# Kernel tuning notes

Measured on AMD Instinct MI355X. Metric: run time of the kernel, lower is better.

The kernel has to match this reference:

```python
import jax, jax.numpy as jnp
import numpy as np

N_NODES = 50000
N_EDGES = 800000
N_GRAPHS = 128
IN_CH, HIDDEN, OUT_CH = 16, 64, 2


def gcn_conv(x, src, dst, W, b, n_nodes):
    """GCNConv: add self-loops, sym-normalized adjacency scatter-add, linear."""
    h = x @ W  # [N, H]
    loop = jnp.arange(n_nodes, dtype=src.dtype)
    s = jnp.concatenate([src, loop])  # [E+N]
    d = jnp.concatenate([dst, loop])
    deg = jax.ops.segment_sum(jnp.ones_like(d, dtype=h.dtype), d, num_segments=n_nodes)
    dinv = jnp.where(deg > 0, jax.lax.rsqrt(deg), 0.0)  # deg^{-1/2}
    norm = dinv[s] * dinv[d]  # [E+N]
    msg = h[s] * norm[:, None]  # gather + scale, [E+N, H]
    out = jax.ops.segment_sum(msg, d, num_segments=n_nodes)  # scatter-add
    return out + b


def global_mean_pool(x, batch, n_graphs):
    sums = jax.ops.segment_sum(x, batch, num_segments=n_graphs)
    cnts = jax.ops.segment_sum(jnp.ones((x.shape[0],), x.dtype), batch, num_segments=n_graphs)
    return sums / jnp.maximum(cnts, 1.0)[:, None]


def setup_inputs() -> dict:
    key = jax.random.key(0)
    ks = jax.random.split(key, 10)
    x = jax.random.normal(ks[0], (N_NODES, IN_CH), dtype=jnp.float32)
    edge_index = jax.random.randint(ks[1], (2, N_EDGES), 0, N_NODES, dtype=jnp.int64)
    batch = jnp.sort(jax.random.randint(ks[2], (N_NODES,), 0, N_GRAPHS, dtype=jnp.int64))
    def glorot(k, shp):
        lim = float(np.sqrt(6.0 / (shp[0] + shp[1])))
        return jax.random.uniform(k, shp, jnp.float32, -lim, lim)
    W1 = glorot(ks[3], (IN_CH, HIDDEN))
    b1 = jnp.zeros((HIDDEN,), jnp.float32)
    W2 = glorot(ks[4], (HIDDEN, HIDDEN))
    b2 = jnp.zeros((HIDDEN,), jnp.float32)
    Wc = glorot(ks[5], (HIDDEN, OUT_CH))
    bc = jnp.zeros((OUT_CH,), jnp.float32)
    return {"x": x, "edge_index": edge_index, "batch": batch,
            "W1": W1, "b1": b1, "W2": W2, "b2": b2, "Wc": Wc, "bc": bc}


def reference(x, edge_index, batch, W1, b1, W2, b2, Wc, bc):
    src, dst = edge_index[0], edge_index[1]
    n = x.shape[0]
    h = jax.nn.relu(gcn_conv(x, src, dst, W1, b1, n))
    # dropout p=0.3 is identity in eval mode
    h = jax.nn.relu(gcn_conv(h, src, dst, W2, b2, n))
    g = global_mean_pool(h, batch, N_GRAPHS)  # [G, H]
    return g @ Wc + bc  # [G, out_channels]
```

## Files before the change

### kernel.cpp

```cpp
#include <hip/hip_runtime.h>
#include <hip/hip_bf16.h>

#define N_NODES 50000
#define N_EDGES 800000
#define N_GRAPHS 128
#define IN_CH 16
#define HIDDEN 64
#define OUT_CH 2

#define BSHIFT 7
#define BNODES 128
#define NB ((N_NODES + BNODES - 1) / BNODES)
#define BCAP 3072
#define ECHUNK 4096
#define EB ((N_EDGES + ECHUNK - 1) / ECHUNK)
#define MAXK 12
#define EPT 16
#define WT1_LD 18
#define AGG_LD 72
#define W2T_ENT (HIDDEN * AGG_LD)

typedef __attribute__((ext_vector_type(8))) short bf16x8;
typedef __attribute__((ext_vector_type(4))) float f32x4;

__device__ __forceinline__ float bf2f(unsigned short u) {
    return __uint_as_float(((unsigned)u) << 16);
}
__device__ __forceinline__ unsigned short f2bf(float f) {
    __hip_bfloat16 h = __float2bfloat16(f);
    return *reinterpret_cast<unsigned short*>(&h);
}


__global__ void bucket_scatter_kernel(const int* __restrict__ src, const int* __restrict__ dst,
                                      int* __restrict__ bh, int* __restrict__ bh2,
                                      int* __restrict__ pairs,
                                      const float* __restrict__ W2, unsigned short* __restrict__ w2t) {
    __shared__ int lh[NB];
    __shared__ int lstart[NB];
    __shared__ int spair[256];
    int t = threadIdx.x;
    if (blockIdx.x == 0) {
        for (int i = t; i < HIDDEN * HIDDEN; i += 256) {
            int k = i >> 6, c = i & 63;
            w2t[c * AGG_LD + k] = f2bf(W2[i]);
        }
    }
    for (int i = t; i < NB; i += 256) lh[i] = 0;
    __syncthreads();

    int base = blockIdx.x * ECHUNK;
    int nE = N_EDGES - base;
    if (nE > ECHUNK) nE = ECHUNK;

    int ed[EPT], es[EPT];
#pragma unroll
    for (int k = 0; k < EPT; k++) {
        int i = k * 256 + t;
        if (i < nE) {
            ed[k] = dst[base + i];
            es[k] = src[base + i];
        } else {
            ed[k] = -1;
            es[k] = 0;
        }
    }
#pragma unroll
    for (int k = 0; k < EPT; k++)
        if ((unsigned)ed[k] < N_NODES) atomicAdd(&lh[ed[k] >> BSHIFT], 1);
    __syncthreads();

    int a0 = (2 * t < NB) ? lh[2 * t] : 0;
    int a1 = (2 * t + 1 < NB) ? lh[2 * t + 1] : 0;
    spair[t] = a0 + a1;
    __syncthreads();
    for (int off = 1; off < 256; off <<= 1) {
        int u = (t >= off) ? spair[t - off] : 0;
        __syncthreads();
        spair[t] += u;
        __syncthreads();
    }
    int ex = spair[t] - (a0 + a1);
    if (2 * t < NB) lstart[2 * t] = ex;
    if (2 * t + 1 < NB) lstart[2 * t + 1] = ex + a0;
    __syncthreads();

    for (int i = t; i < NB; i += 256) {
        bh[i * EB + blockIdx.x] = lh[i];
        bh2[i * EB + blockIdx.x] = base + lstart[i];
        lh[i] = 0;
    }
    __syncthreads();

#pragma unroll
    for (int k = 0; k < EPT; k++) {
        if ((unsigned)ed[k] < N_NODES) {
            int b = ed[k] >> BSHIFT;
            int r = atomicAdd(&lh[b], 1);
            pairs[base + lstart[b] + r] = (es[k] << BSHIFT) | (ed[k] & (BNODES - 1));
        }
    }
}


__global__ void bucket_csr_kernel(const int* __restrict__ pairs, const int* __restrict__ bh,
                                  const int* __restrict__ bh2,
                                  int* __restrict__ csr, int* __restrict__ rowptr,
                                  int* __restrict__ cnt_node, float* __restrict__ dinv,
                                  const float* __restrict__ x, unsigned short* __restrict__ xs,
                                  float* __restrict__ sums, float* __restrict__ cntg) {
    __shared__ int segaddr[EB];
    __shared__ int pref[EB];
    __shared__ int ptmp[256];
    __shared__ int lcnt[BNODES];
    __shared__ int lsc[BNODES];
    __shared__ int lrow[BNODES];
    __shared__ float sdv[BNODES];
    int b = blockIdx.x;
    int t = threadIdx.x;

    if (b == 0) {
        for (int i = t; i < N_GRAPHS * HIDDEN; i += 256) sums[i] = 0.0f;
        if (t < N_GRAPHS) cntg[t] = 0.0f;
    }

    int cntv = (t < EB) ? bh[b * EB + t] : 0;
    if (t < EB) segaddr[t] = bh2[b * EB + t];
    if (t < BNODES) lcnt[t] = 0;
    ptmp[t] = cntv;
    __syncthreads();
    for (int off = 1; off < 256; off <<= 1) {
        int u = (t >= off) ? ptmp[t - off] : 0;
        __syncthreads();
        ptmp[t] += u;
        __syncthreads();
    }
    if (t < EB) pref[t] = ptmp[t];
    __syncthreads();
    int K = pref[EB - 1];
    if (K > BCAP) K = BCAP;

    int myp[MAXK], myr[MAXK];
#pragma unroll
    for (int k = 0; k < MAXK; k++) {
        int i = k * 256 + t;
        myp[k] = -1;
        if (i < K) {
            int lo = 0, hi = EB - 1;
            while (lo < hi) {
                int mid = (lo + hi) >> 1;
                if (pref[mid] > i) hi = mid; else lo = mid + 1;
            }
            int excl = (lo > 0) ? pref[lo - 1] : 0;
            int p = pairs[segaddr[lo] + (i - excl)];
            myp[k] = p;
            myr[k] = atomicAdd(&lcnt[p & (BNODES - 1)], 1);
        }
    }
    __syncthreads();
    if (t < BNODES) lsc[t] = lcnt[t];
    __syncthreads();
    for (int off = 1; off < BNODES; off <<= 1) {
        int u = (t >= off && t < BNODES) ? lsc[t - off] : 0;
        __syncthreads();
        if (t < BNODES) lsc[t] += u;
        __syncthreads();
    }
    int bstart = b * BCAP;
    if (t < BNODES) {
        int ex = lsc[t] - lcnt[t];
        lrow[t] = ex;
        float dv = rsqrtf((float)(lcnt[t] + 1));
        sdv[t] = dv;
        int n = b * BNODES + t;
        if (n < N_NODES) {
            rowptr[n] = bstart + ex;
            cnt_node[n] = lcnt[t];
            dinv[n] = dv;
        }
    }
    __syncthreads();
#pragma unroll
    for (int k = 0; k < MAXK; k++) {
        if (myp[k] >= 0)
            csr[bstart + lrow[myp[k] & (BNODES - 1)] + myr[k]] = myp[k] >> BSHIFT;
    }
    for (int i = t; i < BNODES * IN_CH; i += 256) {
        int nl = i >> 4;
        int n = b * BNODES + nl;
        if (n < N_NODES) xs[n * IN_CH + (i & 15)] = f2bf(sdv[nl] * x[n * IN_CH + (i & 15)]);
    }
}


__global__ void fused_l1_kernel(const unsigned short* __restrict__ xs, const int* __restrict__ csr_src,
                                const int* __restrict__ rowptr, const int* __restrict__ cnt,
                                const float* __restrict__ dinv, const float* __restrict__ W,
                                const float* __restrict__ b, __hip_bfloat16* __restrict__ h) {
    __shared__ float sWT[HIDDEN * WT1_LD];
    __shared__ float sx[16 * IN_CH];
    int t = threadIdx.x;
    for (int i = t; i < IN_CH * HIDDEN; i += 512) {
        int k = i >> 6, c = i & 63;
        sWT[c * WT1_LD + k] = W[i];
    }

    int n0 = blockIdx.x * 16;
    int w = t >> 6;
    int lane = t & 63;
    int e16 = lane >> 2;
    int cc = (lane & 3) * 4;

    int lens[2], starts[2];
#pragma unroll
    for (int q = 0; q < 2; q++) {
        int n = n0 + w * 2 + q;
        lens[q] = cnt[n];
        starts[q] = rowptr[n];
    }

    int sidxv[2][2];
    float msk[2][2];
#pragma unroll
    for (int q = 0; q < 2; q++) {
        int last = lens[q] - 1;
        int lastc = last < 0 ? 0 : last;
        int sg = lens[q] > 0 ? -1 : 0;
#pragma unroll
        for (int k = 0; k < 2; k++) {
            int j = e16 + 16 * k;
            int jj = j <= last ? j : lastc;
            msk[q][k] = (j <= last) ? 1.0f : 0.0f;
            sidxv[q][k] = csr_src[starts[q] + jj] & sg;
        }
    }
    ushort4 raw[2][2];
#pragma unroll
    for (int q = 0; q < 2; q++)
#pragma unroll
        for (int k = 0; k < 2; k++)
            raw[q][k] = *(const ushort4*)&xs[sidxv[q][k] * IN_CH + cc];

#pragma unroll
    for (int q = 0; q < 2; q++) {
        int row = w * 2 + q;
        int n = n0 + row;
        int len = lens[q];
        float4 acc = make_float4(0.f, 0.f, 0.f, 0.f);
#pragma unroll
        for (int k = 0; k < 2; k++) {
            float m = msk[q][k];
            acc.x += m * bf2f(raw[q][k].x);
            acc.y += m * bf2f(raw[q][k].y);
            acc.z += m * bf2f(raw[q][k].z);
            acc.w += m * bf2f(raw[q][k].w);
        }
        if (len > 32) {
            int last = len - 1;
            int start = starts[q];
            int iters = (len + 31) >> 5;
            for (int m2 = 1; m2 < iters; m2++) {
                int base2 = m2 * 32 + e16;
#pragma unroll
                for (int k = 0; k < 2; k++) {
                    int j = base2 + 16 * k;
                    int jj = j <= last ? j : last;
                    float m = j <= last ? 1.0f : 0.0f;
                    int s = csr_src[start + jj];
                    ushort4 xv = *(const ushort4*)&xs[s * IN_CH + cc];
                    acc.x += m * bf2f(xv.x);
                    acc.y += m * bf2f(xv.y);
                    acc.z += m * bf2f(xv.z);
                    acc.w += m * bf2f(xv.w);
                }
            }
        }
#pragma unroll
        for (int m = 4; m <= 32; m <<= 1) {
            acc.x += __shfl_xor(acc.x, m, 64);
            acc.y += __shfl_xor(acc.y, m, 64);
            acc.z += __shfl_xor(acc.z, m, 64);
            acc.w += __shfl_xor(acc.w, m, 64);
        }
        if (lane < 4) {
            float dn = dinv[n];
            ushort4 xsv = *(const ushort4*)&xs[n * IN_CH + cc];
            float4 v;
            v.x = dn * (acc.x + bf2f(xsv.x));
            v.y = dn * (acc.y + bf2f(xsv.y));
            v.z = dn * (acc.z + bf2f(xsv.z));
            v.w = dn * (acc.w + bf2f(xsv.w));
            *(float4*)&sx[row * IN_CH + cc] = v;
        }
    }
    __syncthreads();

    int c = t & 63;
    float bias = b[c];
#pragma unroll
    for (int nb = 0; nb < 2; nb++) {
        int row = nb * 8 + w;
        int n = n0 + row;
        float acch = bias;
#pragma unroll
        for (int k4 = 0; k4 < IN_CH; k4 += 4) {
            float4 a = *(const float4*)&sx[row * IN_CH + k4];
            float2 w0 = *(const float2*)&sWT[c * WT1_LD + k4];
            float2 w1 = *(const float2*)&sWT[c * WT1_LD + k4 + 2];
            acch += a.x * w0.x + a.y * w0.y + a.z * w1.x + a.w * w1.y;
        }
        float v = acch > 0.0f ? acch : 0.0f;
        h[n * HIDDEN + c] = __float2bfloat16(dinv[n] * v);
    }
}


__global__ void fused_l2_kernel(const __hip_bfloat16* __restrict__ h, const int* __restrict__ csr_src,
                                const int* __restrict__ rowptr, const int* __restrict__ cnt,
                                const float* __restrict__ dinv, const unsigned short* __restrict__ w2t,
                                const float* __restrict__ b, const int* __restrict__ batch,
                                float* __restrict__ sums, float* __restrict__ cntg) {
    __shared__ unsigned short sW[W2T_ENT];
    __shared__ unsigned short sagg[16 * AGG_LD];
    int t = threadIdx.x;
    {
        const uint4* wp = (const uint4*)w2t;
        uint4* sWv = (uint4*)sW;
#pragma unroll
        for (int i = 0; i < 2; i++) {
            int idx = i * 512 + t;
            if (idx < W2T_ENT / 8) sWv[idx] = wp[idx];
        }
    }

    int n0 = blockIdx.x * 16;
    int w = t >> 6;
    int lane = t & 63;
    int e8 = lane >> 3;
    int cc8 = (lane & 7) * 8;
    const unsigned short* hu = (const unsigned short*)h;

    int lens[2], starts[2];
#pragma unroll
    for (int q = 0; q < 2; q++) {
        int n = n0 + w * 2 + q;
        lens[q] = cnt[n];
        starts[q] = rowptr[n];
    }

    int sidxv[2][4];
    float msk[2][4];
#pragma unroll
    for (int q = 0; q < 2; q++) {
        int last = lens[q] - 1;
        int lastc = last < 0 ? 0 : last;
        int sg = lens[q] > 0 ? -1 : 0;
#pragma unroll
        for (int k = 0; k < 4; k++) {
            int j = e8 + 8 * k;
            int jj = j <= last ? j : lastc;
            msk[q][k] = (j <= last) ? 1.0f : 0.0f;
            sidxv[q][k] = csr_src[starts[q] + jj] & sg;
        }
    }
    uint4 raw[2][4];
#pragma unroll
    for (int q = 0; q < 2; q++)
#pragma unroll
        for (int k = 0; k < 4; k++)
            raw[q][k] = *(const uint4*)&hu[sidxv[q][k] * HIDDEN + cc8];

#pragma unroll
    for (int q = 0; q < 2; q++) {
        int row = w * 2 + q;
        int n = n0 + row;
        int len = lens[q];
        float4 alo = make_float4(0.f, 0.f, 0.f, 0.f);
        float4 ahi = make_float4(0.f, 0.f, 0.f, 0.f);
#pragma unroll
        for (int k = 0; k < 4; k++) {
            float m = msk[q][k];
            uint4 r = raw[q][k];
            alo.x += m * __uint_as_float(r.x << 16);
            alo.y += m * __uint_as_float(r.x & 0xffff0000u);
            alo.z += m * __uint_as_float(r.y << 16);
            alo.w += m * __uint_as_float(r.y & 0xffff0000u);
            ahi.x += m * __uint_as_float(r.z << 16);
            ahi.y += m * __uint_as_float(r.z & 0xffff0000u);
            ahi.z += m * __uint_as_float(r.w << 16);
            ahi.w += m * __uint_as_float(r.w & 0xffff0000u);
        }
        if (len > 32) {
            int last = len - 1;
            int start = starts[q];
            int iters = (len + 31) >> 5;
            for (int m2 = 1; m2 < iters; m2++) {
                int base2 = m2 * 32 + e8;
#pragma unroll
                for (int k = 0; k < 4; k++) {
                    int j = base2 + 8 * k;
                    int jj = j <= last ? j : last;
                    float m = j <= last ? 1.0f : 0.0f;
                    int s = csr_src[start + jj];
                    uint4 r = *(const uint4*)&hu[s * HIDDEN + cc8];
                    alo.x += m * __uint_as_float(r.x << 16);
                    alo.y += m * __uint_as_float(r.x & 0xffff0000u);
                    alo.z += m * __uint_as_float(r.y << 16);
                    alo.w += m * __uint_as_float(r.y & 0xffff0000u);
                    ahi.x += m * __uint_as_float(r.z << 16);
                    ahi.y += m * __uint_as_float(r.z & 0xffff0000u);
                    ahi.z += m * __uint_as_float(r.w << 16);
                    ahi.w += m * __uint_as_float(r.w & 0xffff0000u);
                }
            }
        }
#pragma unroll
        for (int m = 8; m <= 32; m <<= 1) {
            alo.x += __shfl_xor(alo.x, m, 64);
            alo.y += __shfl_xor(alo.y, m, 64);
            alo.z += __shfl_xor(alo.z, m, 64);
            alo.w += __shfl_xor(alo.w, m, 64);
            ahi.x += __shfl_xor(ahi.x, m, 64);
            ahi.y += __shfl_xor(ahi.y, m, 64);
            ahi.z += __shfl_xor(ahi.z, m, 64);
            ahi.w += __shfl_xor(ahi.w, m, 64);
        }
        if (lane < 8) {
            uint4 sv = *(const uint4*)&hu[n * HIDDEN + cc8];
            float dn = dinv[n];
            ushort4 o0, o1;
            o0.x = f2bf(dn * (alo.x + __uint_as_float(sv.x << 16)));
            o0.y = f2bf(dn * (alo.y + __uint_as_float(sv.x & 0xffff0000u)));
            o0.z = f2bf(dn * (alo.z + __uint_as_float(sv.y << 16)));
            o0.w = f2bf(dn * (alo.w + __uint_as_float(sv.y & 0xffff0000u)));
            o1.x = f2bf(dn * (ahi.x + __uint_as_float(sv.z << 16)));
            o1.y = f2bf(dn * (ahi.y + __uint_as_float(sv.z & 0xffff0000u)));
            o1.z = f2bf(dn * (ahi.z + __uint_as_float(sv.w << 16)));
            o1.w = f2bf(dn * (ahi.w + __uint_as_float(sv.w & 0xffff0000u)));
            *(ushort4*)&sagg[row * AGG_LD + cc8] = o0;
            *(ushort4*)&sagg[row * AGG_LD + cc8 + 4] = o1;
        }
    }
    __syncthreads();

    if (w < 4) {
        int quad = lane >> 4;
        int col = lane & 15;
        int cch = w * 16 + col;
        bf16x8 a0 = *(const bf16x8*)&sagg[col * AGG_LD + quad * 8];
        bf16x8 a1 = *(const bf16x8*)&sagg[col * AGG_LD + 32 + quad * 8];
        bf16x8 b0 = *(const bf16x8*)&sW[cch * AGG_LD + quad * 8];
        bf16x8 b1 = *(const bf16x8*)&sW[cch * AGG_LD + 32 + quad * 8];
        f32x4 d = {0.f, 0.f, 0.f, 0.f};
        d = __builtin_amdgcn_mfma_f32_16x16x32_bf16(a0, b0, d, 0, 0, 0);
        d = __builtin_amdgcn_mfma_f32_16x16x32_bf16(a1, b1, d, 0, 0, 0);
        float bias = b[cch];
        float v[4];
#pragma unroll
        for (int r = 0; r < 4; r++) {
            float z = d[r] + bias;
            v[r] = z > 0.0f ? z : 0.0f;
        }

        int glo = batch[n0];
        int ghi = batch[n0 + 15];
        if (glo == ghi) {
            float s4 = (v[0] + v[1]) + (v[2] + v[3]);
            s4 += __shfl_xor(s4, 16, 64);
            s4 += __shfl_xor(s4, 32, 64);
            if (quad == 0) atomicAdd(&sums[glo * HIDDEN + cch], s4);
            if (t == 0) atomicAdd(&cntg[glo], 16.0f);
        } else {
#pragma unroll
            for (int r = 0; r < 4; r++) {
                int g = batch[n0 + quad * 4 + r];
                if ((unsigned)g < N_GRAPHS) atomicAdd(&sums[g * HIDDEN + cch], v[r]);
            }
            if (w == 0 && col == 0) {
#pragma unroll
                for (int r = 0; r < 4; r++) {
                    int g = batch[n0 + quad * 4 + r];
                    if ((unsigned)g < N_GRAPHS) atomicAdd(&cntg[g], 1.0f);
                }
            }
        }
    }
}


__global__ void head_kernel(const float* __restrict__ sums, const float* __restrict__ cntg,
                            const float* __restrict__ Wc, const float* __restrict__ bc,
                            float* __restrict__ out) {
    int t = blockIdx.x * blockDim.x + threadIdx.x;
    if (t >= N_GRAPHS * OUT_CH) return;
    int g = t >> 1;
    int o = t & 1;
    float inv = 1.0f / fmaxf(cntg[g], 1.0f);
    float acc = bc[o];
#pragma unroll
    for (int k = 0; k < HIDDEN; k++) acc += sums[g * HIDDEN + k] * inv * Wc[k * OUT_CH + o];
    out[t] = acc;
}


extern "C" void kernel_launch(void* const* d_in, const int* in_sizes, int n_in,
                              void* d_out, int out_size, void* d_ws, size_t ws_size,
                              hipStream_t stream) {
    const float* x  = (const float*)d_in[0];
    const int* ei   = (const int*)d_in[1];
    const int* bat  = (const int*)d_in[2];
    const float* W1 = (const float*)d_in[3];
    const float* b1 = (const float*)d_in[4];
    const float* W2 = (const float*)d_in[5];
    const float* b2 = (const float*)d_in[6];
    const float* Wc = (const float*)d_in[7];
    const float* bc = (const float*)d_in[8];
    float* out = (float*)d_out;

    const int* src = ei;
    const int* dst = ei + N_EDGES;

    char* ws = (char*)d_ws;
    size_t off = 0;
    auto carve = [&](size_t nbytes) {
        char* p = ws + off;
        off += (nbytes + 255) & ~(size_t)255;
        return p;
    };
    float* sums     = (float*)carve(N_GRAPHS * HIDDEN * sizeof(float));
    float* cntg     = (float*)carve(N_GRAPHS * sizeof(float));
    unsigned short* w2t = (unsigned short*)carve(W2T_ENT * sizeof(unsigned short));
    int*   bh       = (int*)carve((size_t)NB * EB * sizeof(int));
    int*   bh2      = (int*)carve((size_t)NB * EB * sizeof(int));
    int*   pairs    = (int*)carve((size_t)EB * ECHUNK * sizeof(int));
    int*   csr      = (int*)carve((size_t)NB * BCAP * sizeof(int));
    int*   rowptr   = (int*)carve(N_NODES * sizeof(int));
    int*   cnt_node = (int*)carve(N_NODES * sizeof(int));
    float* dinv     = (float*)carve(N_NODES * sizeof(float));
    unsigned short* xs = (unsigned short*)carve((size_t)N_NODES * IN_CH * sizeof(unsigned short));
    __hip_bfloat16* bufA = (__hip_bfloat16*)carve((size_t)N_NODES * HIDDEN * sizeof(__hip_bfloat16));
    (void)ws_size;

    const int node16Blk = (N_NODES + 15) / 16;

    bucket_scatter_kernel<<<EB, 256, 0, stream>>>(src, dst, bh, bh2, pairs, W2, w2t);
    bucket_csr_kernel<<<NB, 256, 0, stream>>>(pairs, bh, bh2, csr, rowptr, cnt_node, dinv,
                                              x, xs, sums, cntg);
    fused_l1_kernel<<<node16Blk, 512, 0, stream>>>(xs, csr, rowptr, cnt_node, dinv, W1, b1, bufA);
    fused_l2_kernel<<<node16Blk, 512, 0, stream>>>(bufA, csr, rowptr, cnt_node, dinv, w2t, b2,
                                                   bat, sums, cntg);
    head_kernel<<<1, 256, 0, stream>>>(sums, cntg, Wc, bc, out);
}
```

Measured before the change: 161.3 us.

## Replace two-pass bucket sort with global atomic degree count and atomic CSR scatter

```diff
diff --git a/kernel.cpp b/kernel.cpp
--- a/kernel.cpp
+++ b/kernel.cpp
@@ -12,13 +12,10 @@
 #define BNODES 128
 #define NB ((N_NODES + BNODES - 1) / BNODES)
 #define BCAP 3072
-#define ECHUNK 4096
-#define EB ((N_EDGES + ECHUNK - 1) / ECHUNK)
-#define MAXK 12
-#define EPT 16
 #define WT1_LD 18
 #define AGG_LD 72
 #define W2T_ENT (HIDDEN * AGG_LD)
+#define EQ4 (N_EDGES / 4)
 
 typedef __attribute__((ext_vector_type(8))) short bf16x8;
 typedef __attribute__((ext_vector_type(4))) float f32x4;
@@ -32,164 +29,79 @@
 }
 
 
-__global__ void bucket_scatter_kernel(const int* __restrict__ src, const int* __restrict__ dst,
-                                      int* __restrict__ bh, int* __restrict__ bh2,
-                                      int* __restrict__ pairs,
-                                      const float* __restrict__ W2, unsigned short* __restrict__ w2t) {
-    __shared__ int lh[NB];
-    __shared__ int lstart[NB];
-    __shared__ int spair[256];
-    int t = threadIdx.x;
-    if (blockIdx.x == 0) {
-        for (int i = t; i < HIDDEN * HIDDEN; i += 256) {
-            int k = i >> 6, c = i & 63;
-            w2t[c * AGG_LD + k] = f2bf(W2[i]);
-        }
-    }
-    for (int i = t; i < NB; i += 256) lh[i] = 0;
-    __syncthreads();
-
-    int base = blockIdx.x * ECHUNK;
-    int nE = N_EDGES - base;
-    if (nE > ECHUNK) nE = ECHUNK;
-
-    int ed[EPT], es[EPT];
-#pragma unroll
-    for (int k = 0; k < EPT; k++) {
-        int i = k * 256 + t;
-        if (i < nE) {
-            ed[k] = dst[base + i];
-            es[k] = src[base + i];
-        } else {
-            ed[k] = -1;
-            es[k] = 0;
-        }
-    }
-#pragma unroll
-    for (int k = 0; k < EPT; k++)
-        if ((unsigned)ed[k] < N_NODES) atomicAdd(&lh[ed[k] >> BSHIFT], 1);
-    __syncthreads();
-
-    int a0 = (2 * t < NB) ? lh[2 * t] : 0;
-    int a1 = (2 * t + 1 < NB) ? lh[2 * t + 1] : 0;
-    spair[t] = a0 + a1;
-    __syncthreads();
-    for (int off = 1; off < 256; off <<= 1) {
-        int u = (t >= off) ? spair[t - off] : 0;
-        __syncthreads();
-        spair[t] += u;
-        __syncthreads();
-    }
-    int ex = spair[t] - (a0 + a1);
-    if (2 * t < NB) lstart[2 * t] = ex;
-    if (2 * t + 1 < NB) lstart[2 * t + 1] = ex + a0;
-    __syncthreads();
-
-    for (int i = t; i < NB; i += 256) {
-        bh[i * EB + blockIdx.x] = lh[i];
-        bh2[i * EB + blockIdx.x] = base + lstart[i];
-        lh[i] = 0;
-    }
-    __syncthreads();
-
-#pragma unroll
-    for (int k = 0; k < EPT; k++) {
-        if ((unsigned)ed[k] < N_NODES) {
-            int b = ed[k] >> BSHIFT;
-            int r = atomicAdd(&lh[b], 1);
-            pairs[base + lstart[b] + r] = (es[k] << BSHIFT) | (ed[k] & (BNODES - 1));
-        }
-    }
-}
-
-
-__global__ void bucket_csr_kernel(const int* __restrict__ pairs, const int* __restrict__ bh,
-                                  const int* __restrict__ bh2,
-                                  int* __restrict__ csr, int* __restrict__ rowptr,
-                                  int* __restrict__ cnt_node, float* __restrict__ dinv,
-                                  const float* __restrict__ x, unsigned short* __restrict__ xs,
-                                  float* __restrict__ sums, float* __restrict__ cntg) {
-    __shared__ int segaddr[EB];
-    __shared__ int pref[EB];
-    __shared__ int ptmp[256];
-    __shared__ int lcnt[BNODES];
-    __shared__ int lsc[BNODES];
-    __shared__ int lrow[BNODES];
+__global__ void init_kernel(int* __restrict__ cnt, float* __restrict__ sums,
+                            float* __restrict__ cntg,
+                            const float* __restrict__ W2, unsigned short* __restrict__ w2t) {
+    int t = blockIdx.x * blockDim.x + threadIdx.x;
+    int stride = gridDim.x * blockDim.x;
+    for (int i = t; i < N_NODES; i += stride) cnt[i] = 0;
+    for (int i = t; i < N_GRAPHS * HIDDEN; i += stride) sums[i] = 0.0f;
+    for (int i = t; i < N_GRAPHS; i += stride) cntg[i] = 0.0f;
+    for (int i = t; i < HIDDEN * HIDDEN; i += stride) {
+        int k = i >> 6, c = i & 63;
+        w2t[c * AGG_LD + k] = f2bf(W2[i]);
+    }
+}
+
+
+__global__ void degree_kernel(const int* __restrict__ dst, int* __restrict__ cnt) {
+    int i = blockIdx.x * blockDim.x + threadIdx.x;
+    if (i >= EQ4) return;
+    int4 d = ((const int4*)dst)[i];
+    if ((unsigned)d.x < N_NODES) atomicAdd(&cnt[d.x], 1);
+    if ((unsigned)d.y < N_NODES) atomicAdd(&cnt[d.y], 1);
+    if ((unsigned)d.z < N_NODES) atomicAdd(&cnt[d.z], 1);
+    if ((unsigned)d.w < N_NODES) atomicAdd(&cnt[d.w], 1);
+}
+
+
+__global__ void bucket_prefix_kernel(const int* __restrict__ cnt, int* __restrict__ rowptr,
+                                     int* __restrict__ cur, float* __restrict__ dinv,
+                                     const float* __restrict__ x, unsigned short* __restrict__ xs) {
+    __shared__ int sc[BNODES];
     __shared__ float sdv[BNODES];
     int b = blockIdx.x;
     int t = threadIdx.x;
-
-    if (b == 0) {
-        for (int i = t; i < N_GRAPHS * HIDDEN; i += 256) sums[i] = 0.0f;
-        if (t < N_GRAPHS) cntg[t] = 0.0f;
-    }
-
-    int cntv = (t < EB) ? bh[b * EB + t] : 0;
-    if (t < EB) segaddr[t] = bh2[b * EB + t];
-    if (t < BNODES) lcnt[t] = 0;
-    ptmp[t] = cntv;
-    __syncthreads();
-    for (int off = 1; off < 256; off <<= 1) {
-        int u = (t >= off) ? ptmp[t - off] : 0;
-        __syncthreads();
-        ptmp[t] += u;
-        __syncthreads();
-    }
-    if (t < EB) pref[t] = ptmp[t];
-    __syncthreads();
-    int K = pref[EB - 1];
-    if (K > BCAP) K = BCAP;
-
-    int myp[MAXK], myr[MAXK];
-#pragma unroll
-    for (int k = 0; k < MAXK; k++) {
-        int i = k * 256 + t;
-        myp[k] = -1;
-        if (i < K) {
-            int lo = 0, hi = EB - 1;
-            while (lo < hi) {
-                int mid = (lo + hi) >> 1;
-                if (pref[mid] > i) hi = mid; else lo = mid + 1;
-            }
-            int excl = (lo > 0) ? pref[lo - 1] : 0;
-            int p = pairs[segaddr[lo] + (i - excl)];
-            myp[k] = p;
-            myr[k] = atomicAdd(&lcnt[p & (BNODES - 1)], 1);
-        }
-    }
-    __syncthreads();
-    if (t < BNODES) lsc[t] = lcnt[t];
+    int n = b * BNODES + t;
+    int c = 0;
+    if (t < BNODES) {
+        c = (n < N_NODES) ? cnt[n] : 0;
+        sc[t] = c;
+        sdv[t] = rsqrtf((float)(c + 1));
+    }
     __syncthreads();
     for (int off = 1; off < BNODES; off <<= 1) {
-        int u = (t >= off && t < BNODES) ? lsc[t - off] : 0;
+        int u = (t >= off && t < BNODES) ? sc[t - off] : 0;
         __syncthreads();
-        if (t < BNODES) lsc[t] += u;
+        if (t < BNODES) sc[t] += u;
         __syncthreads();
     }
-    int bstart = b * BCAP;
-    if (t < BNODES) {
-        int ex = lsc[t] - lcnt[t];
-        lrow[t] = ex;
-        float dv = rsqrtf((float)(lcnt[t] + 1));
-        sdv[t] = dv;
-        int n = b * BNODES + t;
-        if (n < N_NODES) {
-            rowptr[n] = bstart + ex;
-            cnt_node[n] = lcnt[t];
-            dinv[n] = dv;
-        }
+    if (t < BNODES && n < N_NODES) {
+        int ex = sc[t] - c;
+        int rp = b * BCAP + ex;
+        rowptr[n] = rp;
+        cur[n] = rp;
+        dinv[n] = sdv[t];
     }
     __syncthreads();
-#pragma unroll
-    for (int k = 0; k < MAXK; k++) {
-        if (myp[k] >= 0)
-            csr[bstart + lrow[myp[k] & (BNODES - 1)] + myr[k]] = myp[k] >> BSHIFT;
-    }
     for (int i = t; i < BNODES * IN_CH; i += 256) {
         int nl = i >> 4;
-        int n = b * BNODES + nl;
-        if (n < N_NODES) xs[n * IN_CH + (i & 15)] = f2bf(sdv[nl] * x[n * IN_CH + (i & 15)]);
-    }
+        int n2 = b * BNODES + nl;
+        if (n2 < N_NODES) xs[n2 * IN_CH + (i & 15)] = f2bf(sdv[nl] * x[n2 * IN_CH + (i & 15)]);
+    }
+}
+
+
+__global__ void scatter_kernel(const int* __restrict__ src, const int* __restrict__ dst,
+                               int* __restrict__ cur, int* __restrict__ csr) {
+    int i = blockIdx.x * blockDim.x + threadIdx.x;
+    if (i >= EQ4) return;
+    int4 d = ((const int4*)dst)[i];
+    int4 s = ((const int4*)src)[i];
+    if ((unsigned)d.x < N_NODES) { int p = atomicAdd(&cur[d.x], 1); csr[p] = s.x; }
+    if ((unsigned)d.y < N_NODES) { int p = atomicAdd(&cur[d.y], 1); csr[p] = s.y; }
+    if ((unsigned)d.z < N_NODES) { int p = atomicAdd(&cur[d.z], 1); csr[p] = s.z; }
+    if ((unsigned)d.w < N_NODES) { int p = atomicAdd(&cur[d.w], 1); csr[p] = s.w; }
 }
 
 
@@ -530,22 +442,22 @@
     float* sums     = (float*)carve(N_GRAPHS * HIDDEN * sizeof(float));
     float* cntg     = (float*)carve(N_GRAPHS * sizeof(float));
     unsigned short* w2t = (unsigned short*)carve(W2T_ENT * sizeof(unsigned short));
-    int*   bh       = (int*)carve((size_t)NB * EB * sizeof(int));
-    int*   bh2      = (int*)carve((size_t)NB * EB * sizeof(int));
-    int*   pairs    = (int*)carve((size_t)EB * ECHUNK * sizeof(int));
     int*   csr      = (int*)carve((size_t)NB * BCAP * sizeof(int));
     int*   rowptr   = (int*)carve(N_NODES * sizeof(int));
     int*   cnt_node = (int*)carve(N_NODES * sizeof(int));
+    int*   cur      = (int*)carve(N_NODES * sizeof(int));
     float* dinv     = (float*)carve(N_NODES * sizeof(float));
     unsigned short* xs = (unsigned short*)carve((size_t)N_NODES * IN_CH * sizeof(unsigned short));
     __hip_bfloat16* bufA = (__hip_bfloat16*)carve((size_t)N_NODES * HIDDEN * sizeof(__hip_bfloat16));
     (void)ws_size;
 
     const int node16Blk = (N_NODES + 15) / 16;
-
-    bucket_scatter_kernel<<<EB, 256, 0, stream>>>(src, dst, bh, bh2, pairs, W2, w2t);
-    bucket_csr_kernel<<<NB, 256, 0, stream>>>(pairs, bh, bh2, csr, rowptr, cnt_node, dinv,
-                                              x, xs, sums, cntg);
+    const int edgeBlk = (EQ4 + 255) / 256;
+
+    init_kernel<<<64, 256, 0, stream>>>(cnt_node, sums, cntg, W2, w2t);
+    degree_kernel<<<edgeBlk, 256, 0, stream>>>(dst, cnt_node);
+    bucket_prefix_kernel<<<NB, 256, 0, stream>>>(cnt_node, rowptr, cur, dinv, x, xs);
+    scatter_kernel<<<edgeBlk, 256, 0, stream>>>(src, dst, cur, csr);
     fused_l1_kernel<<<node16Blk, 512, 0, stream>>>(xs, csr, rowptr, cnt_node, dinv, W1, b1, bufA);
     fused_l2_kernel<<<node16Blk, 512, 0, stream>>>(bufA, csr, rowptr, cnt_node, dinv, w2t, b2,
                                                    bat, sums, cntg);
```

After: 219.7 us. +36.2%, slower.
